# Kernel optimization log

Measured on AMD Instinct MI355X. Metric: run time of the kernel, lower is better.

Reference implementation:

```python
import jax, jax.numpy as jnp
import numpy as np

NUM_MEMORIES = 4096
FEATURES = 4096
NUM_HEADS = 16
THRESHOLD = 1.0 / NUM_MEMORIES
EPSILON = 1e-12
COS_EPS = 1e-8
ENTROPY_COEF = 0.0002


def setup_inputs() -> dict:
    key = jax.random.key(0)
    ks = jax.random.split(key, 10)
    B, C, H, W = 256, 256, 4, 4
    F = FEATURES
    bound = float(np.sqrt(6.0 / F))  # kaiming_uniform fan_in = features
    x = jax.random.normal(ks[0], (B, C, H, W), dtype=jnp.float32)
    memory = jax.random.uniform(ks[1], (NUM_MEMORIES, F), minval=-bound, maxval=bound, dtype=jnp.float32)
    s = 0.02
    Wq = jax.random.normal(ks[2], (F, F), dtype=jnp.float32) * s
    Wk = jax.random.normal(ks[3], (F, F), dtype=jnp.float32) * s
    Wv = jax.random.normal(ks[4], (F, F), dtype=jnp.float32) * s
    Wo = jax.random.normal(ks[5], (F, F), dtype=jnp.float32) * s
    bq = jax.random.normal(ks[6], (F,), dtype=jnp.float32) * s
    bk = jax.random.normal(ks[7], (F,), dtype=jnp.float32) * s
    bv = jax.random.normal(ks[8], (F,), dtype=jnp.float32) * s
    bo = jax.random.normal(ks[9], (F,), dtype=jnp.float32) * s
    return {"x": x, "memory": memory, "Wq": Wq, "bq": bq, "Wk": Wk, "bk": bk,
            "Wv": Wv, "bv": bv, "Wo": Wo, "bo": bo}


def _mha(z, Wq, bq, Wk, bk, Wv, bv, Wo, bo):
    # z: [B, C, F] with C == 1 (seq_len = 1 here)
    B, C, F = z.shape
    dk = F // NUM_HEADS
    q = (z @ Wq + bq).reshape(B, C, NUM_HEADS, dk).transpose(0, 2, 1, 3)
    k = (z @ Wk + bk).reshape(B, C, NUM_HEADS, dk).transpose(0, 2, 1, 3)
    v = (z @ Wv + bv).reshape(B, C, NUM_HEADS, dk).transpose(0, 2, 1, 3)
    scores = jnp.einsum('bhqd,bhkd->bhqk', q, k) / jnp.sqrt(jnp.float32(dk))
    w = jax.nn.softmax(scores, axis=-1)
    o = jnp.einsum('bhqk,bhkd->bhqd', w, v).transpose(0, 2, 1, 3).reshape(B, C, F)
    return o @ Wo + bo


def reference(x, memory, Wq, bq, Wk, bk, Wv, bv, Wo, bo):
    B = x.shape[0]
    z = x.reshape(B, -1)[:, None, :]                      # [B, 1, F]
    z = _mha(z, Wq, bq, Wk, bk, Wv, bv, Wo, bo)[:, 0, :]  # [B, F]
    # cosine similarity against memory rows (torch eps = 1e-8, clamped per-vector)
    zn = jnp.maximum(jnp.linalg.norm(z, axis=1), COS_EPS)        # [B]
    mn = jnp.maximum(jnp.linalg.norm(memory, axis=1), COS_EPS)   # [M]
    mem_logit = (z @ memory.T) / (zn[:, None] * mn[None, :])     # [B, M]
    mem_weight = jax.nn.softmax(mem_logit, axis=1)
    # sparse shrinkage: relu(w - t) * w / (|w - t| + eps), then L1 renorm
    d = mem_weight - THRESHOLD
    mem_weight = jax.nn.relu(d) * mem_weight / (jnp.abs(d) + EPSILON)
    mem_weight = mem_weight / jnp.maximum(jnp.sum(jnp.abs(mem_weight), axis=1, keepdims=True), EPSILON)
    z_hat = (mem_weight @ memory).reshape(x.shape)
    entropy = -mem_weight * jnp.log(mem_weight + EPSILON)
    mem_loss = (entropy.sum() / B) * ENTROPY_COEF
    return (z_hat, mem_loss)
```

## Files before the change

kernel.cpp:

```cpp
#include <hip/hip_runtime.h>
#include <math.h>

#define MB 256
#define FF 4096

typedef __attribute__((ext_vector_type(8))) short short8v;
typedef __attribute__((ext_vector_type(4))) short short4v;
typedef __attribute__((ext_vector_type(16))) float f32x16;

__device__ __forceinline__ unsigned short bf16_rne(float f) {
    unsigned u = __builtin_bit_cast(unsigned, f);
    u += 0x7fffu + ((u >> 16) & 1u);
    return (unsigned short)(u >> 16);
}
__device__ __forceinline__ float bf16_f(unsigned short h) {
    unsigned u = ((unsigned)h) << 16;
    return __builtin_bit_cast(float, u);
}
__device__ __forceinline__ size_t apack_idx(int m, int k) {
    return ((size_t)(m >> 5) << 17) + ((size_t)(k >> 3) << 8)
         + ((m & 31) << 3) + (k & 7);
}

__device__ __forceinline__ float block_reduce_sum(float v, float* red) {
    const int tid = threadIdx.x;
    red[tid] = v; __syncthreads();
    for (int s = 128; s > 0; s >>= 1) {
        if (tid < s) red[tid] += red[tid + s];
        __syncthreads();
    }
    float r = red[0]; __syncthreads();
    return r;
}
__device__ __forceinline__ float block_reduce_max(float v, float* red) {
    const int tid = threadIdx.x;
    red[tid] = v; __syncthreads();
    for (int s = 128; s > 0; s >>= 1) {
        if (tid < s) red[tid] = fmaxf(red[tid], red[tid + s]);
        __syncthreads();
    }
    float r = red[0]; __syncthreads();
    return r;
}

__global__ __launch_bounds__(256) void rownorm_kernel(
    const float* __restrict__ src, float* __restrict__ dst, int ncols)
{
    __shared__ float red[256];
    const int row = blockIdx.x, tid = threadIdx.x;
    const float4* p = (const float4*)(src + (size_t)row * ncols);
    float s = 0.f;
    for (int i = tid; i < ncols / 4; i += 256) {
        float4 v = p[i];
        s += v.x * v.x + v.y * v.y + v.z * v.z + v.w * v.w;
    }
    float tot = block_reduce_sum(s, red);
    if (tid == 0) dst[row] = fmaxf(sqrtf(tot), 1e-8f);
}

__global__ __launch_bounds__(256) void split_plain(
    const float* __restrict__ src, unsigned short* __restrict__ hi,
    unsigned short* __restrict__ lo)
{
    const size_t i4 = (size_t)blockIdx.x * 256 + threadIdx.x;
    const size_t base = i4 * 4;
    const int m = (int)(base >> 12), k = (int)(base & 4095);
    const float4 v = *(const float4*)(src + base);
    unsigned short h0 = bf16_rne(v.x), h1 = bf16_rne(v.y), h2 = bf16_rne(v.z), h3 = bf16_rne(v.w);
    const size_t po = apack_idx(m, k);
    short4v hv = { (short)h0, (short)h1, (short)h2, (short)h3 };
    *(short4v*)(hi + po) = hv;
    short4v lv = { (short)bf16_rne(v.x - bf16_f(h0)), (short)bf16_rne(v.y - bf16_f(h1)),
                   (short)bf16_rne(v.z - bf16_f(h2)), (short)bf16_rne(v.w - bf16_f(h3)) };
    *(short4v*)(lo + po) = lv;
}

template <int BSRC, int SPLIT>
__global__ __launch_bounds__(512, 4) void gemm_sk(
    const unsigned short* __restrict__ Ah, const unsigned short* __restrict__ Al,
    const float* __restrict__ B, float* __restrict__ part)
{
    constexpr int PLANES = SPLIT ? 2 : 1;
    constexpr int BUFBYTES = PLANES * 8192;
    __shared__ char Bs[2 * BUFBYTES];

    const int tid = threadIdx.x;
    const int lane = tid & 63, w = tid >> 6;
    const int wm = w >> 1, wn = w & 1;
    const int bn0 = blockIdx.x * 128;
    const int k0 = blockIdx.z * 512;
    const int l31 = lane & 31;

    const float* bsrc;
    int gslot;
    if constexpr (BSRC == 0) {
        const int tk8 = tid >> 7, tn = tid & 127;
        bsrc = B + (size_t)(k0 + tk8 * 8) * FF + bn0 + tn;
        gslot = tid;
    } else {
        const int tn = tid >> 2, tk8 = tid & 3;
        bsrc = B + (size_t)(bn0 + tn) * FF + k0 + tk8 * 8;
        gslot = tk8 * 128 + tn;
    }

    float rB0, rB1, rB2, rB3, rB4, rB5, rB6, rB7;
    float sB0, sB1, sB2, sB3, sB4, sB5, sB6, sB7;

#define LOADB(S, T_)                                                          \
    {                                                                         \
        if constexpr (BSRC == 0) {                                            \
            const float* p_ = bsrc + (size_t)(T_) * 32 * FF;                  \
            S##B0 = p_[0 * FF]; S##B1 = p_[1 * FF];                           \
            S##B2 = p_[2 * FF]; S##B3 = p_[3 * FF];                           \
            S##B4 = p_[4 * FF]; S##B5 = p_[5 * FF];                           \
            S##B6 = p_[6 * FF]; S##B7 = p_[7 * FF];                           \
        } else {                                                              \
            const float* p_ = bsrc + (T_) * 32;                               \
            const float4 f0_ = *(const float4*)p_;                            \
            const float4 f1_ = *(const float4*)(p_ + 4);                      \
            S##B0 = f0_.x; S##B1 = f0_.y; S##B2 = f0_.z; S##B3 = f0_.w;       \
            S##B4 = f1_.x; S##B5 = f1_.y; S##B6 = f1_.z; S##B7 = f1_.w;       \
        }                                                                     \
    }

#define WRITEB(S, BUF_)                                                       \
    {                                                                         \
        unsigned short h0_ = bf16_rne(S##B0), h1_ = bf16_rne(S##B1),          \
                       h2_ = bf16_rne(S##B2), h3_ = bf16_rne(S##B3),          \
                       h4_ = bf16_rne(S##B4), h5_ = bf16_rne(S##B5),          \
                       h6_ = bf16_rne(S##B6), h7_ = bf16_rne(S##B7);          \
        short8v hv_ = { (short)h0_, (short)h1_, (short)h2_, (short)h3_,       \
                        (short)h4_, (short)h5_, (short)h6_, (short)h7_ };     \
        *(short8v*)(Bs + (BUF_) * BUFBYTES + gslot * 16) = hv_;               \
        if constexpr (SPLIT) {                                                \
            short8v lv_ = { (short)bf16_rne(S##B0 - bf16_f(h0_)),             \
                            (short)bf16_rne(S##B1 - bf16_f(h1_)),             \
                            (short)bf16_rne(S##B2 - bf16_f(h2_)),             \
                            (short)bf16_rne(S##B3 - bf16_f(h3_)),             \
                            (short)bf16_rne(S##B4 - bf16_f(h4_)),             \
                            (short)bf16_rne(S##B5 - bf16_f(h5_)),             \
                            (short)bf16_rne(S##B6 - bf16_f(h6_)),             \
                            (short)bf16_rne(S##B7 - bf16_f(h7_)) };           \
            *(short8v*)(Bs + (BUF_) * BUFBYTES + 8192 + gslot * 16) = lv_;    \
        }                                                                     \
    }

    const char* const fragbase =
        (const char*)Bs + (((lane >> 5) * 128) + wn * 64 + l31) * 16;
#define BFRAG(BUF_, P_, KH_, NS_)                                             \
    (*(const short8v*)(fragbase + (BUF_) * BUFBYTES + (P_) * 8192 + (KH_) * 4096 + (NS_) * 512))

    const size_t abase = ((size_t)(blockIdx.y * 4 + wm) << 17)
                       + ((size_t)blockIdx.z << 14)
                       + ((lane >> 5) << 8) + (l31 << 3);
    const unsigned short* pAh = Ah + abase;
    const unsigned short* pAl = SPLIT ? (Al + abase) : pAh;

    short8v cA_h0, cA_h1, cA_l0, cA_l1;
    short8v nA_h0, nA_h1, nA_l0, nA_l1;

#define LOADA(SET, T_)                                                        \
    {                                                                         \
        const int o_ = (T_) * 1024;                                           \
        SET##_h0 = *(const short8v*)(pAh + o_);                               \
        SET##_h1 = *(const short8v*)(pAh + o_ + 512);                         \
        if constexpr (SPLIT) {                                                \
            SET##_l0 = *(const short8v*)(pAl + o_);                           \
            SET##_l1 = *(const short8v*)(pAl + o_ + 512);                     \
        }                                                                     \
    }

    f32x16 acc0 = 0.0f, acc1 = 0.0f;

#define MFMA(A_, B_, C_) C_ = __builtin_amdgcn_mfma_f32_32x32x16_bf16(A_, B_, C_, 0, 0, 0)
#define MMKS(SET, BUF_, KH_)                                                  \
    {                                                                         \
        short8v bh0 = BFRAG(BUF_, 0, KH_, 0);                                 \
        short8v bh1 = BFRAG(BUF_, 0, KH_, 1);                                 \
        MFMA(SET##_h##KH_, bh0, acc0); MFMA(SET##_h##KH_, bh1, acc1);         \
        if constexpr (SPLIT) {                                                \
            short8v bl0 = BFRAG(BUF_, 1, KH_, 0);                             \
            short8v bl1 = BFRAG(BUF_, 1, KH_, 1);                             \
            MFMA(SET##_h##KH_, bl0, acc0); MFMA(SET##_h##KH_, bl1, acc1);     \
            MFMA(SET##_l##KH_, bh0, acc0); MFMA(SET##_l##KH_, bh1, acc1);     \
        }                                                                     \
    }

    LOADB(r, 0)
    LOADA(cA, 0)
    WRITEB(r, 0)
    __syncthreads();

#pragma unroll
    for (int tp = 0; tp < 8; ++tp) {
        const int t = tp * 2;
        LOADB(s, t + 1)
        LOADA(nA, t + 1)
        __builtin_amdgcn_s_setprio(1);
        MMKS(cA, 0, 0)
        MMKS(cA, 0, 1)
        __builtin_amdgcn_s_setprio(0);
        WRITEB(s, 1)
        __syncthreads();
        if (tp < 7) { LOADB(r, t + 2) LOADA(cA, t + 2) }
        __builtin_amdgcn_s_setprio(1);
        MMKS(nA, 1, 0)
        MMKS(nA, 1, 1)
        __builtin_amdgcn_s_setprio(0);
        if (tp < 7) { WRITEB(r, 0) }
        __syncthreads();
    }
#undef LOADB
#undef WRITEB
#undef BFRAG
#undef LOADA
#undef MFMA
#undef MMKS

    float* pp = part + (size_t)blockIdx.z * (MB * FF);
    const int rbase = blockIdx.y * 128 + wm * 32 + 4 * (lane >> 5);
    const int c0 = bn0 + wn * 64 + l31;
#pragma unroll
    for (int r = 0; r < 16; ++r) {
        const int row0 = rbase + (r & 3) + 8 * (r >> 2);
        float* rp0 = pp + (size_t)row0 * FF + c0;
        rp0[0]  = acc0[r];
        rp0[32] = acc1[r];
    }
}

template <int MODE>
__global__ __launch_bounds__(256) void reduce_k(
    const float* __restrict__ part, const float* __restrict__ bias,
    unsigned short* __restrict__ hi, unsigned short* __restrict__ lo,
    float* __restrict__ fout)
{
    const size_t idx4 = (size_t)blockIdx.x * 256 + threadIdx.x;
    const size_t base = idx4 * 4;
    float s0 = 0.f, s1 = 0.f, s2 = 0.f, s3 = 0.f;
#pragma unroll
    for (int c = 0; c < 8; ++c) {
        const float4 p = *(const float4*)(part + (size_t)c * (MB * FF) + base);
        s0 += p.x; s1 += p.y; s2 += p.z; s3 += p.w;
    }
    const int col = (int)(base & 4095);
    const int row = (int)(base >> 12);
    if constexpr (MODE == 0 || MODE == 1) {
        s0 += bias[col]; s1 += bias[col + 1]; s2 += bias[col + 2]; s3 += bias[col + 3];
        unsigned short h0 = bf16_rne(s0), h1 = bf16_rne(s1), h2 = bf16_rne(s2), h3 = bf16_rne(s3);
        const size_t po = apack_idx(row, col);
        short4v hv = { (short)h0, (short)h1, (short)h2, (short)h3 };
        *(short4v*)(hi + po) = hv;
        short4v lv = { (short)bf16_rne(s0 - bf16_f(h0)), (short)bf16_rne(s1 - bf16_f(h1)),
                       (short)bf16_rne(s2 - bf16_f(h2)), (short)bf16_rne(s3 - bf16_f(h3)) };
        *(short4v*)(lo + po) = lv;
        if constexpr (MODE == 1) {
            float4 o = { s0, s1, s2, s3 };
            *(float4*)(fout + base) = o;
        }
    } else {
        float4 o = { s0, s1, s2, s3 };
        *(float4*)(fout + base) = o;
    }
}

__global__ __launch_bounds__(256) void reduce_softmax(
    const float* __restrict__ part, const float* __restrict__ zn,
    const float* __restrict__ mn, unsigned short* __restrict__ w_hi,
    float* __restrict__ rowent)
{
    constexpr float THRESH = 1.0f / 4096.0f;
    constexpr float EPS = 1e-12f;
    __shared__ float srow[4096];
    __shared__ float red[256];
    const int row = blockIdx.x, tid = threadIdx.x;
    const float zr = zn[row];

    for (int i = tid; i < 1024; i += 256) {
        float s0 = 0.f, s1 = 0.f, s2 = 0.f, s3 = 0.f;
#pragma unroll
        for (int c = 0; c < 8; ++c) {
            const float4 p = *(const float4*)(part + (size_t)c * (MB * FF)
                                              + (size_t)row * FF + i * 4);
            s0 += p.x; s1 += p.y; s2 += p.z; s3 += p.w;
        }
        const float4 mv = *(const float4*)(mn + i * 4);
        float4 o = { s0 / (zr * mv.x), s1 / (zr * mv.y),
                     s2 / (zr * mv.z), s3 / (zr * mv.w) };
        *(float4*)(srow + i * 4) = o;
    }
    __syncthreads();

    float m = -INFINITY;
    for (int i = tid; i < FF; i += 256) m = fmaxf(m, srow[i]);
    m = block_reduce_max(m, red);

    float s = 0.f;
    for (int i = tid; i < FF; i += 256) {
        float e = expf(srow[i] - m);
        srow[i] = e; s += e;
    }
    s = block_reduce_sum(s, red);
    const float inv = 1.0f / s;

    float s2 = 0.f;
    for (int i = tid; i < FF; i += 256) {
        float ww = srow[i] * inv;
        float d = ww - THRESH;
        float w2 = fmaxf(d, 0.f) * ww / (fabsf(d) + EPS);
        srow[i] = w2; s2 += w2;
    }
    __syncthreads();
    s2 = block_reduce_sum(s2, red);
    const float inv2 = 1.0f / fmaxf(s2, EPS);

    float ent = 0.f;
    for (int i0 = tid * 8; i0 < FF; i0 += 2048) {
        unsigned short h[8];
#pragma unroll
        for (int j = 0; j < 8; ++j) {
            float w3 = srow[i0 + j] * inv2;
            h[j] = bf16_rne(w3);
            ent -= w3 * logf(w3 + EPS);
        }
        short8v hv = { (short)h[0], (short)h[1], (short)h[2], (short)h[3],
                       (short)h[4], (short)h[5], (short)h[6], (short)h[7] };
        *(short8v*)(w_hi + apack_idx(row, i0)) = hv;
    }
    ent = block_reduce_sum(ent, red);
    if (tid == 0) rowent[row] = ent;
}

__global__ __launch_bounds__(256) void loss_kernel(
    const float* __restrict__ rowent, float* __restrict__ out)
{
    __shared__ float red[256];
    const int tid = threadIdx.x;
    float tot = block_reduce_sum(rowent[tid], red);
    if (tid == 0) out[0] = (tot / 256.0f) * 0.0002f;
}

extern "C" void kernel_launch(void* const* d_in, const int* in_sizes, int n_in,
                              void* d_out, int out_size, void* d_ws, size_t ws_size,
                              hipStream_t stream)
{
    const float* x   = (const float*)d_in[0];
    const float* mem = (const float*)d_in[1];
    const float* Wv  = (const float*)d_in[6];
    const float* bv  = (const float*)d_in[7];
    const float* Wo  = (const float*)d_in[8];
    const float* bo  = (const float*)d_in[9];
    float* out = (float*)d_out;

    char* ws = (char*)d_ws;
    float*          part  = (float*)(ws + 134217728ull);
    unsigned short* x_hi  = (unsigned short*)(ws + 167772160ull);
    unsigned short* x_lo  = (unsigned short*)(ws + 169869312ull);
    unsigned short* v_hi  = (unsigned short*)(ws + 171966464ull);
    unsigned short* v_lo  = (unsigned short*)(ws + 174063616ull);
    unsigned short* o_hi  = (unsigned short*)(ws + 176160768ull);
    unsigned short* o_lo  = (unsigned short*)(ws + 178257920ull);
    float*          o_f32 = (float*)(ws + 180355072ull);
    unsigned short* w_hi  = (unsigned short*)(ws + 188743680ull);
    float*          zn    = (float*)(ws + 190840832ull);
    float*          mn    = zn + MB;
    float*          rowe  = mn + FF;

    const dim3 blk(256);
    const dim3 blkG(512);
    const dim3 gG(32, 2, 8);
    const int gR = (MB * FF) / (4 * 256);

    split_plain<<<gR, blk, 0, stream>>>(x, x_hi, x_lo);
    rownorm_kernel<<<FF, blk, 0, stream>>>(mem, mn, FF);

    gemm_sk<0, 1><<<gG, blkG, 0, stream>>>(x_hi, x_lo, Wv, part);
    reduce_k<0><<<gR, blk, 0, stream>>>(part, bv, v_hi, v_lo, nullptr);

    gemm_sk<0, 1><<<gG, blkG, 0, stream>>>(v_hi, v_lo, Wo, part);
    reduce_k<1><<<gR, blk, 0, stream>>>(part, bo, o_hi, o_lo, o_f32);

    rownorm_kernel<<<MB, blk, 0, stream>>>(o_f32, zn, FF);
    gemm_sk<1, 1><<<gG, blkG, 0, stream>>>(o_hi, o_lo, mem, part);
    reduce_softmax<<<MB, blk, 0, stream>>>(part, zn, mn, w_hi, rowe);

    gemm_sk<0, 0><<<gG, blkG, 0, stream>>>(w_hi, nullptr, mem, part);
    reduce_k<3><<<gR, blk, 0, stream>>>(part, nullptr, nullptr, nullptr, out);

    loss_kernel<<<1, blk, 0, stream>>>(rowe, out + (size_t)MB * FF);
}
```

Baseline: 183.3 us.

## Fuse split-K reduction into GEMM via last-arriving-block atomic counter

```diff
diff --git a/kernel.cpp b/kernel.cpp
--- a/kernel.cpp
+++ b/kernel.cpp
@@ -75,14 +75,18 @@
     *(short4v*)(lo + po) = lv;
 }
 
-template <int BSRC, int SPLIT>
+template <int BSRC, int SPLIT, int RMODE>
 __global__ __launch_bounds__(512, 4) void gemm_sk(
     const unsigned short* __restrict__ Ah, const unsigned short* __restrict__ Al,
-    const float* __restrict__ B, float* __restrict__ part)
+    const float* __restrict__ B, float* __restrict__ part,
+    const float* __restrict__ bias, unsigned short* __restrict__ hi,
+    unsigned short* __restrict__ lo, float* __restrict__ fout,
+    unsigned* __restrict__ cnt)
 {
     constexpr int PLANES = SPLIT ? 2 : 1;
     constexpr int BUFBYTES = PLANES * 8192;
     __shared__ char Bs[2 * BUFBYTES];
+    __shared__ unsigned oldv;
 
     const int tid = threadIdx.x;
     const int lane = tid & 63, w = tid >> 6;
@@ -227,40 +231,51 @@
         rp0[0]  = acc0[r];
         rp0[32] = acc1[r];
     }
-}
-
-template <int MODE>
-__global__ __launch_bounds__(256) void reduce_k(
-    const float* __restrict__ part, const float* __restrict__ bias,
-    unsigned short* __restrict__ hi, unsigned short* __restrict__ lo,
-    float* __restrict__ fout)
-{
-    const size_t idx4 = (size_t)blockIdx.x * 256 + threadIdx.x;
-    const size_t base = idx4 * 4;
-    float s0 = 0.f, s1 = 0.f, s2 = 0.f, s3 = 0.f;
-#pragma unroll
-    for (int c = 0; c < 8; ++c) {
-        const float4 p = *(const float4*)(part + (size_t)c * (MB * FF) + base);
-        s0 += p.x; s1 += p.y; s2 += p.z; s3 += p.w;
-    }
-    const int col = (int)(base & 4095);
-    const int row = (int)(base >> 12);
-    if constexpr (MODE == 0 || MODE == 1) {
-        s0 += bias[col]; s1 += bias[col + 1]; s2 += bias[col + 2]; s3 += bias[col + 3];
-        unsigned short h0 = bf16_rne(s0), h1 = bf16_rne(s1), h2 = bf16_rne(s2), h3 = bf16_rne(s3);
-        const size_t po = apack_idx(row, col);
-        short4v hv = { (short)h0, (short)h1, (short)h2, (short)h3 };
-        *(short4v*)(hi + po) = hv;
-        short4v lv = { (short)bf16_rne(s0 - bf16_f(h0)), (short)bf16_rne(s1 - bf16_f(h1)),
-                       (short)bf16_rne(s2 - bf16_f(h2)), (short)bf16_rne(s3 - bf16_f(h3)) };
-        *(short4v*)(lo + po) = lv;
-        if constexpr (MODE == 1) {
-            float4 o = { s0, s1, s2, s3 };
-            *(float4*)(fout + base) = o;
+
+    if constexpr (RMODE >= 0) {
+        __threadfence();
+        __syncthreads();
+        if (tid == 0)
+            oldv = atomicAdd(&cnt[blockIdx.y * 32 + blockIdx.x], 1u);
+        __syncthreads();
+        if (oldv == 7u) {
+            __threadfence();
+            const int r0 = blockIdx.y * 128;
+#pragma unroll
+            for (int it = 0; it < 8; ++it) {
+                const int q = it * 512 + tid;
+                const int row = r0 + (q >> 5);
+                const int col = bn0 + (q & 31) * 4;
+                const size_t base = (size_t)row * FF + col;
+                float s0 = 0.f, s1 = 0.f, s2 = 0.f, s3 = 0.f;
+#pragma unroll
+                for (int c = 0; c < 8; ++c) {
+                    const float4 p = *(const float4*)(part + (size_t)c * (MB * FF) + base);
+                    s0 += p.x; s1 += p.y; s2 += p.z; s3 += p.w;
+                }
+                if constexpr (RMODE == 0 || RMODE == 1) {
+                    s0 += bias[col]; s1 += bias[col + 1];
+                    s2 += bias[col + 2]; s3 += bias[col + 3];
+                    unsigned short h0 = bf16_rne(s0), h1 = bf16_rne(s1),
+                                   h2 = bf16_rne(s2), h3 = bf16_rne(s3);
+                    const size_t po = apack_idx(row, col);
+                    short4v hv = { (short)h0, (short)h1, (short)h2, (short)h3 };
+                    *(short4v*)(hi + po) = hv;
+                    short4v lv = { (short)bf16_rne(s0 - bf16_f(h0)),
+                                   (short)bf16_rne(s1 - bf16_f(h1)),
+                                   (short)bf16_rne(s2 - bf16_f(h2)),
+                                   (short)bf16_rne(s3 - bf16_f(h3)) };
+                    *(short4v*)(lo + po) = lv;
+                    if constexpr (RMODE == 1) {
+                        float4 o = { s0, s1, s2, s3 };
+                        *(float4*)(fout + base) = o;
+                    }
+                } else {
+                    float4 o = { s0, s1, s2, s3 };
+                    *(float4*)(fout + base) = o;
+                }
+            }
         }
-    } else {
-        float4 o = { s0, s1, s2, s3 };
-        *(float4*)(fout + base) = o;
     }
 }
 
@@ -353,6 +368,7 @@
     float* out = (float*)d_out;
 
     char* ws = (char*)d_ws;
+    unsigned*       cnt   = (unsigned*)ws;
     float*          part  = (float*)(ws + 134217728ull);
     unsigned short* x_hi  = (unsigned short*)(ws + 167772160ull);
     unsigned short* x_lo  = (unsigned short*)(ws + 169869312ull);
@@ -371,21 +387,24 @@
     const dim3 gG(32, 2, 8);
     const int gR = (MB * FF) / (4 * 256);
 
+    hipMemsetAsync(cnt, 0, 3 * 64 * sizeof(unsigned), stream);
+
     split_plain<<<gR, blk, 0, stream>>>(x, x_hi, x_lo);
     rownorm_kernel<<<FF, blk, 0, stream>>>(mem, mn, FF);
 
-    gemm_sk<0, 1><<<gG, blkG, 0, stream>>>(x_hi, x_lo, Wv, part);
-    reduce_k<0><<<gR, blk, 0, stream>>>(part, bv, v_hi, v_lo, nullptr);
-
-    gemm_sk<0, 1><<<gG, blkG, 0, stream>>>(v_hi, v_lo, Wo, part);
-    reduce_k<1><<<gR, blk, 0, stream>>>(part, bo, o_hi, o_lo, o_f32);
+    gemm_sk<0, 1, 0><<<gG, blkG, 0, stream>>>(x_hi, x_lo, Wv, part,
+                                              bv, v_hi, v_lo, nullptr, cnt);
+
+    gemm_sk<0, 1, 1><<<gG, blkG, 0, stream>>>(v_hi, v_lo, Wo, part,
+                                              bo, o_hi, o_lo, o_f32, cnt + 64);
 
     rownorm_kernel<<<MB, blk, 0, stream>>>(o_f32, zn, FF);
-    gemm_sk<1, 1><<<gG, blkG, 0, stream>>>(o_hi, o_lo, mem, part);
+    gemm_sk<1, 1, -1><<<gG, blkG, 0, stream>>>(o_hi, o_lo, mem, part,
+                                               nullptr, nullptr, nullptr, nullptr, nullptr);
     reduce_softmax<<<MB, blk, 0, stream>>>(part, zn, mn, w_hi, rowe);
 
-    gemm_sk<0, 0><<<gG, blkG, 0, stream>>>(w_hi, nullptr, mem, part);
-    reduce_k<3><<<gR, blk, 0, stream>>>(part, nullptr, nullptr, nullptr, out);
+    gemm_sk<0, 0, 3><<<gG, blkG, 0, stream>>>(w_hi, nullptr, mem, part,
+                                              nullptr, nullptr, nullptr, out, cnt + 128);
 
     loss_kernel<<<1, blk, 0, stream>>>(rowe, out + (size_t)MB * FF);
 }
```

After: 576.2 us. 214% more time.
